# Kernel tuning notes

Measured on AMD Instinct MI355X. Metric: run time of the kernel, lower is better.

The kernel has to match this reference:

```python
import jax, jax.numpy as jnp
import numpy as np

B, S, M = 4, 4096, 2048
LATENT, H, D = 512, 16, 128  # latent_dim, num_heads, hidden_dim (per-head)


def setup_inputs() -> dict:
    key = jax.random.key(0)
    ks = jax.random.split(key, 12)
    sd = lambda fan_in: 1.0 / np.sqrt(fan_in)
    return {
        "x": jax.random.normal(ks[0], (B, S, M), dtype=jnp.float32),
        # k path: down-proj to latent, up-proj to H*D (vmapped Dense pair, slice 0)
        "Wd_k": jax.random.normal(ks[1], (M, LATENT), dtype=jnp.float32) * sd(M),
        "bd_k": jnp.zeros((LATENT,), dtype=jnp.float32),
        "Wu_k": jax.random.normal(ks[2], (LATENT, H * D), dtype=jnp.float32) * sd(LATENT),
        "bu_k": jnp.zeros((H * D,), dtype=jnp.float32),
        # v path (slice 1 of the vmapped params)
        "Wd_v": jax.random.normal(ks[3], (M, LATENT), dtype=jnp.float32) * sd(M),
        "bd_v": jnp.zeros((LATENT,), dtype=jnp.float32),
        "Wu_v": jax.random.normal(ks[4], (LATENT, H * D), dtype=jnp.float32) * sd(LATENT),
        "bu_v": jnp.zeros((H * D,), dtype=jnp.float32),
        # q projection
        "Wq": jax.random.normal(ks[5], (M, H * D), dtype=jnp.float32) * sd(M),
        "bq": jnp.zeros((H * D,), dtype=jnp.float32),
        # output projection
        "Wo": jax.random.normal(ks[6], (H * D, M), dtype=jnp.float32) * sd(H * D),
        "bo": jnp.zeros((M,), dtype=jnp.float32),
    }


def reference(x, Wd_k, bd_k, Wu_k, bu_k, Wd_v, bd_v, Wu_v, bu_v, Wq, bq, Wo, bo):
    b, s, m = x.shape
    # low-rank KV: down-project to latent cache, up-project to heads
    cache_k = x @ Wd_k + bd_k                      # [B,S,L]
    cache_v = x @ Wd_v + bd_v                      # [B,S,L]
    k = (cache_k @ Wu_k + bu_k).reshape(b, s, H, D)
    v = (cache_v @ Wu_v + bu_v).reshape(b, s, H, D)
    q = (x @ Wq + bq).reshape(b, s, H, D)
    # NOTE: source permutes k as (0,1,3,2) on [B,S,H,D] -> scores are per-token
    # head-vs-head [B,S,H,H], softmax over the last (head) axis.
    sim = jnp.einsum("bshd,bsgd->bshg", q, k) * (D ** -0.5)
    attn = jax.nn.softmax(sim, axis=-1)            # [B,S,H,H]
    out = jnp.einsum("bshg,bsgd->bshd", attn, v)   # [B,S,H,D]
    out = out.reshape(b, s, H * D)
    return out @ Wo + bo                           # [B,S,M]
```

## Files before the change

### kernel.cpp

```cpp
#include <hip/hip_runtime.h>

typedef __attribute__((ext_vector_type(8))) short short8v;
typedef __attribute__((ext_vector_type(4))) float f32x4;
typedef __attribute__((ext_vector_type(4))) unsigned int uint4v;

#define GLOBAL_AS(p) ((const __attribute__((address_space(1))) void*)(p))
#define LDS_AS(p)    ((__attribute__((address_space(3))) void*)(p))

__device__ __forceinline__ unsigned short f2bf(float f) {
  unsigned int u = __builtin_bit_cast(unsigned int, f);
  u += 0x7fffu + ((u >> 16) & 1u);
  return (unsigned short)(u >> 16);
}
__device__ __forceinline__ float bf2f(unsigned short u) {
  unsigned int x = ((unsigned int)u) << 16;
  return __builtin_bit_cast(float, x);
}

__global__ __launch_bounds__(256) void transpose_to_bf16(
    const float* __restrict__ src, unsigned short* __restrict__ dst,
    int K, int N, int ntx) {
  __shared__ float tile[32][33];
  const int bx = blockIdx.x % ntx;
  const int by = blockIdx.x / ntx;
  const int tx = threadIdx.x & 31, ty = threadIdx.x >> 5;
  const int k0 = by * 32, n0 = bx * 32;
#pragma unroll
  for (int i = 0; i < 32; i += 8)
    tile[ty + i][tx] = src[(size_t)(k0 + ty + i) * N + n0 + tx];
  __syncthreads();
#pragma unroll
  for (int i = 0; i < 32; i += 8)
    dst[(size_t)(n0 + ty + i) * K + k0 + tx] = f2bf(tile[tx][ty + i]);
}

__global__ __launch_bounds__(256) void cvt_f32_bf16(
    const float* __restrict__ s, unsigned short* __restrict__ d) {
  size_t i = ((size_t)blockIdx.x * 256 + threadIdx.x) * 8;
  f32x4 v0 = *(const f32x4*)(s + i);
  f32x4 v1 = *(const f32x4*)(s + i + 4);
  union U8 { uint4v v; unsigned short us[8]; } o;
  o.us[0] = f2bf(v0.x); o.us[1] = f2bf(v0.y); o.us[2] = f2bf(v0.z); o.us[3] = f2bf(v0.w);
  o.us[4] = f2bf(v1.x); o.us[5] = f2bf(v1.y); o.us[6] = f2bf(v1.z); o.us[7] = f2bf(v1.w);
  *(uint4v*)(d + i) = o.v;
}

__global__ __launch_bounds__(256) void copy_f32(
    const float* __restrict__ s, float* __restrict__ d, int n) {
  int i = blockIdx.x * 256 + threadIdx.x;
  if (i < n) d[i] = s[i];
}

#define BM 128
#define BN 128
#define BK 64

template <int OUT_BF16>
__global__ __launch_bounds__(256) void gemm_bt(
    const unsigned short* __restrict__ A, int lda,
    const unsigned short* __restrict__ Bt, int ldb,
    const float* __restrict__ bias, void* __restrict__ Cp, int ldc,
    int K, int ntn) {
  __shared__ unsigned short Als[BM * BK];
  __shared__ unsigned short Bls[BN * BK];
  const int t = threadIdx.x;
  const int lane = t & 63, wave = t >> 6;
  const int bm = (blockIdx.x / ntn) * BM;
  const int bn = (blockIdx.x % ntn) * BN;
  const int wm = (wave >> 1) * 64, wn = (wave & 1) * 64;
  const int g = lane >> 4, r = lane & 15, swz = r & 7;
  const int srow = t >> 3, sj = t & 7, sswz = srow & 7;

  f32x4 acc[4][4];
#pragma unroll
  for (int i = 0; i < 4; ++i)
#pragma unroll
    for (int j = 0; j < 4; ++j) acc[i][j] = (f32x4){0.f, 0.f, 0.f, 0.f};

  const size_t abase = (size_t)(bm + srow) * lda + (size_t)((sj ^ sswz) << 3);
  const size_t bbase = (size_t)(bn + srow) * ldb + (size_t)((sj ^ sswz) << 3);
  unsigned short* ldsA = &Als[wave * 512];
  unsigned short* ldsB = &Bls[wave * 512];

  for (int k0 = 0; k0 < K; k0 += BK) {
#pragma unroll
    for (int c = 0; c < 4; ++c) {
      __builtin_amdgcn_global_load_lds(GLOBAL_AS(A + abase + (size_t)c * 32 * lda + k0),
                                       LDS_AS(ldsA + c * 2048), 16, 0, 0);
      __builtin_amdgcn_global_load_lds(GLOBAL_AS(Bt + bbase + (size_t)c * 32 * ldb + k0),
                                       LDS_AS(ldsB + c * 2048), 16, 0, 0);
    }
    __syncthreads();
#pragma unroll
    for (int ks = 0; ks < 2; ++ks) {
      short8v af[4], bf[4];
#pragma unroll
      for (int i = 0; i < 4; ++i) {
        const int koff = ((((ks << 2) + g) ^ swz) << 3);
        af[i] = *(const short8v*)&Als[(wm + i * 16 + r) * BK + koff];
        bf[i] = *(const short8v*)&Bls[(wn + i * 16 + r) * BK + koff];
      }
#pragma unroll
      for (int mi = 0; mi < 4; ++mi)
#pragma unroll
        for (int ni = 0; ni < 4; ++ni)
          acc[mi][ni] = __builtin_amdgcn_mfma_f32_16x16x32_bf16(
              af[mi], bf[ni], acc[mi][ni], 0, 0, 0);
    }
    __syncthreads();
  }

#pragma unroll
  for (int ni = 0; ni < 4; ++ni) {
    const int col = bn + wn + ni * 16 + r;
    const float bv = bias[col];
#pragma unroll
    for (int mi = 0; mi < 4; ++mi) {
      const int row0 = bm + wm + mi * 16 + (g << 2);
#pragma unroll
      for (int j = 0; j < 4; ++j) {
        float v = acc[mi][ni][j] + bv;
        if (OUT_BF16)
          ((unsigned short*)Cp)[(size_t)(row0 + j) * ldc + col] = f2bf(v);
        else
          ((float*)Cp)[(size_t)(row0 + j) * ldc + col] = v;
      }
    }
  }
}

__global__ __launch_bounds__(256) void attn_kernel(
    const unsigned short* __restrict__ out1, const unsigned short* __restrict__ kv,
    unsigned short* __restrict__ aout) {
  const int s = blockIdx.x;
  const int t = threadIdx.x;
  __shared__ float qs[16 * 132], ks2[16 * 132], vs[16 * 132];
  __shared__ float attn[256];
  const int h = t >> 4, d0 = (t & 15) * 8;

  union U8 { uint4v v; unsigned short us[8]; };
  U8 qv, kv8, vv;
  qv.v = *(const uint4v*)(out1 + (size_t)s * 3072 + 1024 + t * 8);
  kv8.v = *(const uint4v*)(kv + (size_t)s * 4096 + t * 8);
  vv.v = *(const uint4v*)(kv + (size_t)s * 4096 + 2048 + t * 8);
#pragma unroll
  for (int j = 0; j < 8; ++j) {
    qs[h * 132 + d0 + j] = bf2f(qv.us[j]);
    ks2[h * 132 + d0 + j] = bf2f(kv8.us[j]);
    vs[h * 132 + d0 + j] = bf2f(vv.us[j]);
  }
  __syncthreads();

  const int gg0 = t & 15;
  const f32x4* qrow = (const f32x4*)&qs[h * 132];
  const f32x4* krow = (const f32x4*)&ks2[gg0 * 132];
  float acc = 0.f;
#pragma unroll
  for (int dd = 0; dd < 32; ++dd) {
    f32x4 a4 = qrow[dd], b4 = krow[dd];
    acc += a4.x * b4.x + a4.y * b4.y + a4.z * b4.z + a4.w * b4.w;
  }
  acc *= 0.08838834764831845f;
  float mx = acc;
#pragma unroll
  for (int o = 8; o; o >>= 1) mx = fmaxf(mx, __shfl_xor(mx, o));
  float e = __expf(acc - mx);
  float sm = e;
#pragma unroll
  for (int o = 8; o; o >>= 1) sm += __shfl_xor(sm, o);
  attn[t] = e / sm;
  __syncthreads();

  f32x4 o0 = (f32x4){0.f, 0.f, 0.f, 0.f}, o1 = (f32x4){0.f, 0.f, 0.f, 0.f};
#pragma unroll
  for (int gg = 0; gg < 16; ++gg) {
    const float a = attn[(h << 4) + gg];
    f32x4 v0 = *(const f32x4*)&vs[gg * 132 + d0];
    f32x4 v1 = *(const f32x4*)&vs[gg * 132 + d0 + 4];
    o0 += v0 * a;
    o1 += v1 * a;
  }
  U8 ov;
  ov.us[0] = f2bf(o0.x); ov.us[1] = f2bf(o0.y); ov.us[2] = f2bf(o0.z); ov.us[3] = f2bf(o0.w);
  ov.us[4] = f2bf(o1.x); ov.us[5] = f2bf(o1.y); ov.us[6] = f2bf(o1.z); ov.us[7] = f2bf(o1.w);
  *(uint4v*)(aout + (size_t)s * 2048 + t * 8) = ov.v;
}

extern "C" void kernel_launch(void* const* d_in, const int* in_sizes, int n_in,
                              void* d_out, int out_size, void* d_ws, size_t ws_size,
                              hipStream_t stream) {
  (void)in_sizes; (void)n_in; (void)out_size; (void)ws_size;
  const float* x    = (const float*)d_in[0];
  const float* Wd_k = (const float*)d_in[1];
  const float* bd_k = (const float*)d_in[2];
  const float* Wu_k = (const float*)d_in[3];
  const float* bu_k = (const float*)d_in[4];
  const float* Wd_v = (const float*)d_in[5];
  const float* bd_v = (const float*)d_in[6];
  const float* Wu_v = (const float*)d_in[7];
  const float* bu_v = (const float*)d_in[8];
  const float* Wq   = (const float*)d_in[9];
  const float* bq   = (const float*)d_in[10];
  const float* Wo   = (const float*)d_in[11];
  const float* bo   = (const float*)d_in[12];

  char* ws = (char*)d_ws;
  unsigned short* w1t  = (unsigned short*)(ws);
  unsigned short* w2t  = (unsigned short*)(ws + 12582912);
  unsigned short* w3t  = (unsigned short*)(ws + 16777216);
  float*          b1   = (float*)(ws + 25165824);
  float*          b2   = (float*)(ws + 25178112);
  unsigned short* xb   = (unsigned short*)(ws + 25194496);
  unsigned short* out1 = (unsigned short*)(ws + 92303360);
  unsigned short* kvb  = (unsigned short*)(ws + 192966656);
  unsigned short* attO = xb;

  dim3 blk(256);

  transpose_to_bf16<<<dim3(16 * 64), blk, 0, stream>>>(Wd_k, w1t,               2048, 512, 16);
  transpose_to_bf16<<<dim3(16 * 64), blk, 0, stream>>>(Wd_v, w1t + 512 * 2048,  2048, 512, 16);
  transpose_to_bf16<<<dim3(64 * 64), blk, 0, stream>>>(Wq,   w1t + 1024 * 2048, 2048, 2048, 64);
  transpose_to_bf16<<<dim3(64 * 16), blk, 0, stream>>>(Wu_k, w2t,               512, 2048, 64);
  transpose_to_bf16<<<dim3(64 * 16), blk, 0, stream>>>(Wu_v, w2t + 2048 * 512,  512, 2048, 64);
  transpose_to_bf16<<<dim3(64 * 64), blk, 0, stream>>>(Wo,   w3t,               2048, 2048, 64);

  copy_f32<<<dim3(2), blk, 0, stream>>>(bd_k, b1, 512);
  copy_f32<<<dim3(2), blk, 0, stream>>>(bd_v, b1 + 512, 512);
  copy_f32<<<dim3(8), blk, 0, stream>>>(bq,   b1 + 1024, 2048);
  copy_f32<<<dim3(8), blk, 0, stream>>>(bu_k, b2, 2048);
  copy_f32<<<dim3(8), blk, 0, stream>>>(bu_v, b2 + 2048, 2048);

  cvt_f32_bf16<<<dim3(16384), blk, 0, stream>>>(x, xb);

  gemm_bt<1><<<dim3(128 * 24), blk, 0, stream>>>(xb, 2048, w1t, 2048, b1, out1, 3072, 2048, 24);

  gemm_bt<1><<<dim3(128 * 16), blk, 0, stream>>>(out1, 3072, w2t, 512, b2, kvb, 4096, 512, 16);
  gemm_bt<1><<<dim3(128 * 16), blk, 0, stream>>>(out1 + 512, 3072, w2t + 2048 * 512, 512,
                                                 b2 + 2048, kvb + 2048, 4096, 512, 16);

  attn_kernel<<<dim3(16384), blk, 0, stream>>>(out1, kvb, attO);

  gemm_bt<0><<<dim3(128 * 16), blk, 0, stream>>>(attO, 2048, w3t, 2048, bo, (float*)d_out,
                                                 2048, 2048, 16);
}
```

Measured before the change: 704.0 us.

## Rework GEMM to 256x256 tiles with double-buffered LDS pipeline and merged launches

The bf16 GEMM kernel moves to 512-thread blocks with 256x256 output tiles. A double-buffered LDS prefetch with explicit vmcnt waits lets the next K-tile load overlap MFMA work, and block IDs are remapped across XCDs for locality. The two up-projection GEMMs become one launch that selects the A column offset per output tile, and the five bias copies merge into one kernel. Larger tiles raise register and LDS pressure and cut the number of blocks, which may limit occupancy.

```diff
diff --git a/kernel.cpp b/kernel.cpp
--- a/kernel.cpp
+++ b/kernel.cpp
@@ -6,6 +6,9 @@
 
 #define GLOBAL_AS(p) ((const __attribute__((address_space(1))) void*)(p))
 #define LDS_AS(p)    ((__attribute__((address_space(3))) void*)(p))
+#define WAITV(n) asm volatile("s_waitcnt vmcnt(" #n ")" ::: "memory")
+#define BARRIER() __builtin_amdgcn_s_barrier()
+#define SCHED0() __builtin_amdgcn_sched_barrier(0)
 
 __device__ __forceinline__ unsigned short f2bf(float f) {
   unsigned int u = __builtin_bit_cast(unsigned int, f);
@@ -45,78 +48,114 @@
   *(uint4v*)(d + i) = o.v;
 }
 
-__global__ __launch_bounds__(256) void copy_f32(
-    const float* __restrict__ s, float* __restrict__ d, int n) {
+__global__ __launch_bounds__(256) void fill_bias(
+    const float* __restrict__ bd_k, const float* __restrict__ bd_v,
+    const float* __restrict__ bq, const float* __restrict__ bu_k,
+    const float* __restrict__ bu_v, float* __restrict__ b1, float* __restrict__ b2) {
   int i = blockIdx.x * 256 + threadIdx.x;
-  if (i < n) d[i] = s[i];
-}
-
-#define BM 128
-#define BN 128
-#define BK 64
+  if (i < 512) b1[i] = bd_k[i];
+  else if (i < 1024) b1[i] = bd_v[i - 512];
+  else if (i < 3072) b1[i] = bq[i - 1024];
+  else if (i < 5120) b2[i - 3072] = bu_k[i - 3072];
+  else if (i < 7168) b2[i - 3072] = bu_v[i - 5120];
+}
 
 template <int OUT_BF16>
-__global__ __launch_bounds__(256) void gemm_bt(
-    const unsigned short* __restrict__ A, int lda,
+__global__ __launch_bounds__(512, 2) void gemm_bt(
+    const unsigned short* __restrict__ A, int lda, int nsplit_col, int acol_off,
     const unsigned short* __restrict__ Bt, int ldb,
     const float* __restrict__ bias, void* __restrict__ Cp, int ldc,
     int K, int ntn) {
-  __shared__ unsigned short Als[BM * BK];
-  __shared__ unsigned short Bls[BN * BK];
+  __shared__ unsigned short lds[2][2][256 * 64];
   const int t = threadIdx.x;
   const int lane = t & 63, wave = t >> 6;
-  const int bm = (blockIdx.x / ntn) * BM;
-  const int bn = (blockIdx.x % ntn) * BN;
-  const int wm = (wave >> 1) * 64, wn = (wave & 1) * 64;
-  const int g = lane >> 4, r = lane & 15, swz = r & 7;
-  const int srow = t >> 3, sj = t & 7, sswz = srow & 7;
-
-  f32x4 acc[4][4];
-#pragma unroll
-  for (int i = 0; i < 4; ++i)
+
+  const int q = gridDim.x >> 3;
+  const int bid = (blockIdx.x & 7) * q + (blockIdx.x >> 3);
+  const int bm = (bid / ntn) * 256;
+  const int bn = (bid % ntn) * 256;
+  const unsigned short* Ab = A + (bn >= nsplit_col ? acol_off : 0);
+
+  const int wr = wave >> 2, wc = wave & 3;
+  const int g = lane >> 4, r = lane & 15;
+  const int srow = t >> 3, sj = t & 7;
+  const int jsrc = sj ^ (srow & 7);
+  const int NT = K >> 6;
+
+  f32x4 acc[8][4];
+#pragma unroll
+  for (int i = 0; i < 8; ++i)
 #pragma unroll
     for (int j = 0; j < 4; ++j) acc[i][j] = (f32x4){0.f, 0.f, 0.f, 0.f};
 
-  const size_t abase = (size_t)(bm + srow) * lda + (size_t)((sj ^ sswz) << 3);
-  const size_t bbase = (size_t)(bn + srow) * ldb + (size_t)((sj ^ sswz) << 3);
-  unsigned short* ldsA = &Als[wave * 512];
-  unsigned short* ldsB = &Bls[wave * 512];
-
-  for (int k0 = 0; k0 < K; k0 += BK) {
+  const unsigned short* aptr = Ab + (size_t)(bm + srow) * lda + (jsrc << 3);
+  const unsigned short* bptr = Bt + (size_t)(bn + srow) * ldb + (jsrc << 3);
+  const int sbase = wave * 512;
+
+  auto stage = [&](int kt, int buf) {
+    const unsigned short* ak = aptr + kt * 64;
+    const unsigned short* bk = bptr + kt * 64;
+    unsigned short* la = &lds[buf][0][sbase];
+    unsigned short* lb = &lds[buf][1][sbase];
 #pragma unroll
     for (int c = 0; c < 4; ++c) {
-      __builtin_amdgcn_global_load_lds(GLOBAL_AS(A + abase + (size_t)c * 32 * lda + k0),
-                                       LDS_AS(ldsA + c * 2048), 16, 0, 0);
-      __builtin_amdgcn_global_load_lds(GLOBAL_AS(Bt + bbase + (size_t)c * 32 * ldb + k0),
-                                       LDS_AS(ldsB + c * 2048), 16, 0, 0);
-    }
-    __syncthreads();
+      __builtin_amdgcn_global_load_lds(GLOBAL_AS(ak + (size_t)c * 64 * lda),
+                                       LDS_AS(la + c * 4096), 16, 0, 0);
+      __builtin_amdgcn_global_load_lds(GLOBAL_AS(bk + (size_t)c * 64 * ldb),
+                                       LDS_AS(lb + c * 4096), 16, 0, 0);
+    }
+  };
+
+  stage(0, 0);
+
+  const int arow = wr * 128 + r;
+  const int brow = wc * 64 + r;
+  const int swz = r & 7;
+
+  for (int kt = 0; kt < NT; ++kt) {
+    const int cur = kt & 1;
+    if (kt + 1 < NT) {
+      stage(kt + 1, cur ^ 1);
+      SCHED0();
+      WAITV(8);
+    } else {
+      WAITV(0);
+    }
+    BARRIER();
+    SCHED0();
+    const unsigned short* la = lds[cur][0];
+    const unsigned short* lb = lds[cur][1];
 #pragma unroll
     for (int ks = 0; ks < 2; ++ks) {
-      short8v af[4], bf[4];
-#pragma unroll
-      for (int i = 0; i < 4; ++i) {
-        const int koff = ((((ks << 2) + g) ^ swz) << 3);
-        af[i] = *(const short8v*)&Als[(wm + i * 16 + r) * BK + koff];
-        bf[i] = *(const short8v*)&Bls[(wn + i * 16 + r) * BK + koff];
-      }
-#pragma unroll
-      for (int mi = 0; mi < 4; ++mi)
+      const int c16 = (((ks << 2) + g) ^ swz) << 3;
+      short8v bfr[4], afr[8];
+#pragma unroll
+      for (int ni = 0; ni < 4; ++ni)
+        bfr[ni] = *(const short8v*)&lb[(brow + ni * 16) * 64 + c16];
+#pragma unroll
+      for (int mi = 0; mi < 8; ++mi)
+        afr[mi] = *(const short8v*)&la[(arow + mi * 16) * 64 + c16];
+      __builtin_amdgcn_s_setprio(1);
+#pragma unroll
+      for (int mi = 0; mi < 8; ++mi)
 #pragma unroll
         for (int ni = 0; ni < 4; ++ni)
           acc[mi][ni] = __builtin_amdgcn_mfma_f32_16x16x32_bf16(
-              af[mi], bf[ni], acc[mi][ni], 0, 0, 0);
-    }
-    __syncthreads();
+              afr[mi], bfr[ni], acc[mi][ni], 0, 0, 0);
+      __builtin_amdgcn_s_setprio(0);
+    }
+    SCHED0();
+    BARRIER();
+    SCHED0();
   }
 
 #pragma unroll
   for (int ni = 0; ni < 4; ++ni) {
-    const int col = bn + wn + ni * 16 + r;
+    const int col = bn + wc * 64 + ni * 16 + r;
     const float bv = bias[col];
 #pragma unroll
-    for (int mi = 0; mi < 4; ++mi) {
-      const int row0 = bm + wm + mi * 16 + (g << 2);
+    for (int mi = 0; mi < 8; ++mi) {
+      const int row0 = bm + wr * 128 + mi * 16 + (g << 2);
 #pragma unroll
       for (int j = 0; j < 4; ++j) {
         float v = acc[mi][ni][j] + bv;
@@ -224,22 +263,18 @@
   transpose_to_bf16<<<dim3(64 * 16), blk, 0, stream>>>(Wu_v, w2t + 2048 * 512,  512, 2048, 64);
   transpose_to_bf16<<<dim3(64 * 64), blk, 0, stream>>>(Wo,   w3t,               2048, 2048, 64);
 
-  copy_f32<<<dim3(2), blk, 0, stream>>>(bd_k, b1, 512);
-  copy_f32<<<dim3(2), blk, 0, stream>>>(bd_v, b1 + 512, 512);
-  copy_f32<<<dim3(8), blk, 0, stream>>>(bq,   b1 + 1024, 2048);
-  copy_f32<<<dim3(8), blk, 0, stream>>>(bu_k, b2, 2048);
-  copy_f32<<<dim3(8), blk, 0, stream>>>(bu_v, b2 + 2048, 2048);
+  fill_bias<<<dim3(28), blk, 0, stream>>>(bd_k, bd_v, bq, bu_k, bu_v, b1, b2);
 
   cvt_f32_bf16<<<dim3(16384), blk, 0, stream>>>(x, xb);
 
-  gemm_bt<1><<<dim3(128 * 24), blk, 0, stream>>>(xb, 2048, w1t, 2048, b1, out1, 3072, 2048, 24);
-
-  gemm_bt<1><<<dim3(128 * 16), blk, 0, stream>>>(out1, 3072, w2t, 512, b2, kvb, 4096, 512, 16);
-  gemm_bt<1><<<dim3(128 * 16), blk, 0, stream>>>(out1 + 512, 3072, w2t + 2048 * 512, 512,
-                                                 b2 + 2048, kvb + 2048, 4096, 512, 16);
+  gemm_bt<1><<<dim3(64 * 12), dim3(512), 0, stream>>>(
+      xb, 2048, 1 << 30, 0, w1t, 2048, b1, out1, 3072, 2048, 12);
+
+  gemm_bt<1><<<dim3(64 * 16), dim3(512), 0, stream>>>(
+      out1, 3072, 2048, 512, w2t, 512, b2, kvb, 4096, 512, 16);
 
   attn_kernel<<<dim3(16384), blk, 0, stream>>>(out1, kvb, attO);
 
-  gemm_bt<0><<<dim3(128 * 16), blk, 0, stream>>>(attO, 2048, w3t, 2048, bo, (float*)d_out,
-                                                 2048, 2048, 16);
-}
+  gemm_bt<0><<<dim3(64 * 8), dim3(512), 0, stream>>>(
+      attO, 2048, 1 << 30, 0, w3t, 2048, bo, (float*)d_out, 2048, 2048, 8);
+}
```

Result: faster. 609.3 us (median of 2 runs) (-13.5%).
